# Optimization experiments

Measured on AMD Instinct MI355X. Metric: run time of the kernel, lower is better.

Reference implementation:

```python
import jax, jax.numpy as jnp
import numpy as np

IN_DIM = 1024
HIDDEN = 1024
NUM_HEAD = 16
HEAD_DIM = HIDDEN // NUM_HEAD
B, S = 4, 2048


def setup_inputs() -> dict:
    key = jax.random.key(0)
    ks = jax.random.split(key, 10)
    sc = 1.0 / np.sqrt(IN_DIM)
    inp = {
        "x": jax.random.normal(ks[0], (B, S, IN_DIM), dtype=jnp.float32),
        "mask": jnp.ones((B, 1, 1, S), dtype=jnp.int32),
        "Wq": jax.random.normal(ks[1], (IN_DIM, HIDDEN), dtype=jnp.float32) * sc,
        "bq": jnp.zeros((HIDDEN,), dtype=jnp.float32),
        "Wk": jax.random.normal(ks[2], (IN_DIM, HIDDEN), dtype=jnp.float32) * sc,
        "bk": jnp.zeros((HIDDEN,), dtype=jnp.float32),
        "Wv": jax.random.normal(ks[3], (IN_DIM, HIDDEN), dtype=jnp.float32) * sc,
        "bv": jnp.zeros((HIDDEN,), dtype=jnp.float32),
        "Wo": jax.random.normal(ks[4], (HIDDEN, IN_DIM), dtype=jnp.float32) * sc,
        "bo": jnp.zeros((IN_DIM,), dtype=jnp.float32),
    }
    return inp


def reference(x, mask, Wq, bq, Wk, bk, Wv, bv, Wo, bo):
    Bq, Sq, _ = x.shape
    # projections -> [B, H, S, hd]
    def proj(W, b):
        return (x @ W + b).reshape(Bq, Sq, NUM_HEAD, HEAD_DIM).transpose(0, 2, 1, 3)
    q, k, v = proj(Wq, bq), proj(Wk, bk), proj(Wv, bv)
    scale = 1.0 / jnp.sqrt(jnp.asarray(HEAD_DIM, dtype=x.dtype))
    scores = jnp.einsum("bhqd,bhkd->bhqk", q, k) * scale  # [B,H,S,S]
    scores = jnp.where(mask == 0, jnp.asarray(-1e9, dtype=x.dtype), scores)
    attn = jax.nn.softmax(scores, axis=-1)
    out = jnp.einsum("bhqk,bhkd->bhqd", attn, v)  # [B,H,S,hd]
    out = out.transpose(0, 2, 1, 3).reshape(Bq, Sq, HIDDEN)
    return out @ Wo + bo
```

## Files before the change

### kernel.cpp

```cpp
#include <hip/hip_runtime.h>
#include <hip/hip_bf16.h>
#include <stdint.h>

#define BB_ 4
#define SS_ 2048
#define IND_ 1024
#define HIDD_ 1024
#define NH_ 16
#define HD_ 64

typedef __attribute__((ext_vector_type(8))) short vshort8;
typedef __attribute__((ext_vector_type(4))) short vshort4;
typedef __attribute__((ext_vector_type(4))) float vfloat4;

__device__ __forceinline__ short bf16_of(float f) {
    union { float f; uint32_t u; } v; v.f = f;
    uint32_t r = v.u + 0x7fffu + ((v.u >> 16) & 1u);
    return (short)(r >> 16);
}

__device__ __forceinline__ uint32_t pk_bf16(float lo, float hi) {
    uint32_t r;
    asm("v_cvt_pk_bf16_f32 %0, %1, %2" : "=v"(r) : "v"(lo), "v"(hi));
    return r;
}

typedef const __attribute__((address_space(1))) uint8_t* gas_ptr;
typedef __attribute__((address_space(3))) uint8_t* las_ptr;
__device__ __forceinline__ void gload16(const void* g, void* l) {
    __builtin_amdgcn_global_load_lds((gas_ptr)g, (las_ptr)l, 16, 0, 0);
}

__global__ __launch_bounds__(256) void conv_x(const float* __restrict__ x,
                                              short* __restrict__ xb, int n4) {
    int i = blockIdx.x * 256 + threadIdx.x;
    if (i >= n4) return;
    float4 v = ((const float4*)x)[i];
    vshort4 r;
    r[0] = bf16_of(v.x); r[1] = bf16_of(v.y); r[2] = bf16_of(v.z); r[3] = bf16_of(v.w);
    ((vshort4*)xb)[i] = r;
}

__global__ __launch_bounds__(256) void convT_w4(const float* __restrict__ W0,
                                                const float* __restrict__ W1,
                                                const float* __restrict__ W2,
                                                const float* __restrict__ W3,
                                                short* __restrict__ T0,
                                                short* __restrict__ T1,
                                                short* __restrict__ T2,
                                                short* __restrict__ T3) {
    const float* W = (blockIdx.z == 0) ? W0 : (blockIdx.z == 1) ? W1 : (blockIdx.z == 2) ? W2 : W3;
    short* Wt = (blockIdx.z == 0) ? T0 : (blockIdx.z == 1) ? T1 : (blockIdx.z == 2) ? T2 : T3;
    __shared__ short tile[64][65];
    int k0 = blockIdx.x * 64, n0 = blockIdx.y * 64;
#pragma unroll
    for (int i = 0; i < 16; i++) {
        int idx = i * 256 + threadIdx.x;
        int r = idx >> 6, c = idx & 63;
        tile[c][r] = bf16_of(W[(k0 + r) * 1024 + n0 + c]);
    }
    __syncthreads();
#pragma unroll
    for (int i = 0; i < 16; i++) {
        int idx = i * 256 + threadIdx.x;
        int r = idx >> 6, c = idx & 63;
        Wt[(n0 + r) * 1024 + k0 + c] = tile[r][c];
    }
}

template <int MODE>
__device__ __forceinline__ void gemm_body(const short* __restrict__ A,
                                          const short* __restrict__ Bt,
                                          const float* __restrict__ bias,
                                          void* __restrict__ out, float scale,
                                          short* smem) {
    constexpr int Kd = 1024;
    const int t = threadIdx.x;
    const int w = t >> 6, lane = t & 63;
    const int g = lane >> 4, c = lane & 15;
    const int wm = w >> 1, wn = w & 1;
    const int m0 = blockIdx.x * 128, n0 = blockIdx.y * 128;

    const int row = t >> 2;
    const int colE = (t & 3) * 8;

    const short* ga0 = A + (size_t)(m0 + row) * Kd + colE;
    const short* ga1 = A + (size_t)(m0 + 64 + row) * Kd + colE;
    const short* gb0 = Bt + (size_t)(n0 + row) * Kd + colE;
    const short* gb1 = Bt + (size_t)(n0 + 64 + row) * Kd + colE;

    vfloat4 acc[4][4] = {};

    gload16(ga0, &smem[t * 8]);
    gload16(ga1, &smem[2048 + t * 8]);
    gload16(gb0, &smem[4096 + t * 8]);
    gload16(gb1, &smem[6144 + t * 8]);
    __syncthreads();

    for (int k0 = 0; k0 < Kd; k0 += 32) {
        const int cur = (k0 >> 5) & 1;
        const int nb = (cur ^ 1) * 8192;
        if (k0 + 32 < Kd) {
            gload16(ga0 + k0 + 32, &smem[nb + t * 8]);
            gload16(ga1 + k0 + 32, &smem[nb + 2048 + t * 8]);
            gload16(gb0 + k0 + 32, &smem[nb + 4096 + t * 8]);
            gload16(gb1 + k0 + 32, &smem[nb + 6144 + t * 8]);
        }
        const int cb = cur * 8192;
        vshort8 af[4], bfr[4];
#pragma unroll
        for (int mi = 0; mi < 4; mi++)
            af[mi] = *(const vshort8*)&smem[cb + (wm * 64 + mi * 16 + c) * 32 + g * 8];
#pragma unroll
        for (int ni = 0; ni < 4; ni++)
            bfr[ni] = *(const vshort8*)&smem[cb + 4096 + (wn * 64 + ni * 16 + c) * 32 + g * 8];
#pragma unroll
        for (int mi = 0; mi < 4; mi++)
#pragma unroll
            for (int ni = 0; ni < 4; ni++)
                acc[mi][ni] = __builtin_amdgcn_mfma_f32_16x16x32_bf16(
                    af[mi], bfr[ni], acc[mi][ni], 0, 0, 0);
        __syncthreads();
    }

#pragma unroll
    for (int ni = 0; ni < 4; ni++) {
        const int n = n0 + wn * 64 + ni * 16 + c;
        const float bv = bias[n];
#pragma unroll
        for (int mi = 0; mi < 4; mi++) {
#pragma unroll
            for (int r = 0; r < 4; r++) {
                const int m = m0 + wm * 64 + mi * 16 + g * 4 + r;
                const float v = (acc[mi][ni][r] + bv) * scale;
                if (MODE == 0) {
                    const int b = m >> 11, s = m & 2047, h = n >> 6, d = n & 63;
                    ((short*)out)[(((size_t)(b * 16 + h)) * 2048 + s) * 64 + d] = bf16_of(v);
                } else {
                    ((float*)out)[(size_t)m * 1024 + n] = v;
                }
            }
        }
    }
}

__global__ __launch_bounds__(256) void gemm_qkv(const short* __restrict__ xb,
                                                const short* __restrict__ Wqt,
                                                const short* __restrict__ Wkt,
                                                const short* __restrict__ Wvt,
                                                const float* __restrict__ bq,
                                                const float* __restrict__ bk,
                                                const float* __restrict__ bv,
                                                short* __restrict__ Qb,
                                                short* __restrict__ Kb,
                                                short* __restrict__ Vb) {
    __shared__ alignas(16) short smem[16384];
    const int z = blockIdx.z;
    const short* Bt = (z == 0) ? Wqt : (z == 1) ? Wkt : Wvt;
    const float* bias = (z == 0) ? bq : (z == 1) ? bk : bv;
    short* out = (z == 0) ? Qb : (z == 1) ? Kb : Vb;
    const float scale = (z == 0) ? 0.125f * 1.4426950408889634f : 1.0f;
    gemm_body<0>(xb, Bt, bias, out, scale, smem);
}

__global__ __launch_bounds__(256) void gemm_out(const short* __restrict__ A,
                                                const short* __restrict__ Bt,
                                                const float* __restrict__ bias,
                                                float* __restrict__ out) {
    __shared__ alignas(16) short smem[16384];
    gemm_body<1>(A, Bt, bias, out, 1.0f, smem);
}

__global__ __launch_bounds__(256) void transpose_v(const short* __restrict__ V,
                                                   short* __restrict__ Vt) {
    __shared__ short tile[64][65];
    const int bh = blockIdx.y;
    const int s0 = blockIdx.x * 64;
#pragma unroll
    for (int i = 0; i < 16; i++) {
        int idx = i * 256 + threadIdx.x;
        int r = idx >> 6, c = idx & 63;
        tile[c][r] = V[((size_t)bh * 2048 + s0 + r) * 64 + c];
    }
    __syncthreads();
#pragma unroll
    for (int i = 0; i < 16; i++) {
        int idx = i * 256 + threadIdx.x;
        int r = idx >> 6, c = idx & 63;
        Vt[((size_t)bh * 64 + r) * 2048 + s0 + c] = tile[r][c];
    }
}

__device__ __forceinline__ vshort8 lds_frag(const short* base, int row, int off) {
    const int byte = row * 128 + (off ^ ((row & 7) << 4));
    return *(const vshort8*)((const char*)base + byte);
}
__device__ __forceinline__ uint2 lds_frag8B(const short* base, int row, int eoff) {
    const int byte = row * 128 + ((eoff * 2) ^ ((row & 7) << 4));
    return *(const uint2*)((const char*)base + byte);
}
__device__ __forceinline__ void lds_stg(short* base, int row, int e8, vshort8 v) {
    const int byte = row * 128 + ((e8 * 16) ^ ((row & 7) << 4));
    *(vshort8*)((char*)base + byte) = v;
}

__global__ __launch_bounds__(256) void attn_kernel(const short* __restrict__ Q,
                                                   const short* __restrict__ K,
                                                   const short* __restrict__ Vt,
                                                   const int* __restrict__ mask,
                                                   short* __restrict__ Oattn) {
    __shared__ alignas(16) short Kl[2][64 * 64];
    __shared__ alignas(16) short Vl[2][64 * 64];
    const int tid = threadIdx.x, w = tid >> 6, lane = tid & 63;
    const int g = lane >> 4, c = lane & 15;
    const int bh = blockIdx.y, bb = bh >> 4, h = bh & 15;
    const int q0 = blockIdx.x * 128 + w * 32;
    const short* Qb = Q + (size_t)bh * 2048 * 64;
    const short* Kb = K + (size_t)bh * 2048 * 64;
    const short* Vb = Vt + (size_t)bh * 64 * 2048;
    const int* mb = mask + bb * 2048;

    const int srow = tid >> 3, se8 = tid & 7;
    const int srow2 = srow + 32;

    vshort8 qa[2][2];
#pragma unroll
    for (int qt = 0; qt < 2; qt++)
#pragma unroll
        for (int kf = 0; kf < 2; kf++)
            qa[qt][kf] = *(const vshort8*)(Qb + (size_t)(q0 + qt * 16 + c) * 64 + kf * 32 + g * 8);

    vfloat4 o[2][4] = {};
    vfloat4 osum[2] = {};
    const vfloat4 ZF = {0.f, 0.f, 0.f, 0.f};
    vshort8 ONESV;
#pragma unroll
    for (int i = 0; i < 8; i++) ONESV[i] = (short)0x3F80;

    vshort8 rk0 = *(const vshort8*)(Kb + (size_t)srow * 64 + se8 * 8);
    vshort8 rk1 = *(const vshort8*)(Kb + (size_t)srow2 * 64 + se8 * 8);
    vshort8 rv0 = *(const vshort8*)(Vb + (size_t)srow * 2048 + se8 * 8);
    vshort8 rv1 = *(const vshort8*)(Vb + (size_t)srow2 * 2048 + se8 * 8);
    lds_stg(Kl[0], srow, se8, rk0);
    lds_stg(Kl[0], srow2, se8, rk1);
    lds_stg(Vl[0], srow, se8, rv0);
    lds_stg(Vl[0], srow2, se8, rv1);
    __syncthreads();

    for (int t = 0; t < 32; t++) {
        const int k0 = t * 64;
        const short* Kc = Kl[t & 1];
        const short* Vc = Vl[t & 1];
        const bool more = (t + 1 < 32);
        if (more) {
            const int kn = k0 + 64;
            rk0 = *(const vshort8*)(Kb + (size_t)(kn + srow) * 64 + se8 * 8);
            rk1 = *(const vshort8*)(Kb + (size_t)(kn + srow2) * 64 + se8 * 8);
            rv0 = *(const vshort8*)(Vb + (size_t)srow * 2048 + kn + se8 * 8);
            rv1 = *(const vshort8*)(Vb + (size_t)srow2 * 2048 + kn + se8 * 8);
        }

        const int mv = mb[k0 + lane];
        const bool allone = __all(mv != 0);

        vshort8 kb[4][2];
#pragma unroll
        for (int kt = 0; kt < 4; kt++) {
            kb[kt][0] = lds_frag(Kc, kt * 16 + c, g * 16);
            kb[kt][1] = lds_frag(Kc, kt * 16 + c, 64 + g * 16);
        }
        vfloat4 s[2][4];
        __builtin_amdgcn_s_setprio(1);
#pragma unroll
        for (int qt = 0; qt < 2; qt++)
#pragma unroll
            for (int kt = 0; kt < 4; kt++) {
                vfloat4 z = __builtin_amdgcn_mfma_f32_16x16x32_bf16(kb[kt][0], qa[qt][0], ZF, 0, 0, 0);
                s[qt][kt] = __builtin_amdgcn_mfma_f32_16x16x32_bf16(kb[kt][1], qa[qt][1], z, 0, 0, 0);
            }
        __builtin_amdgcn_s_setprio(0);

        if (!allone) {
#pragma unroll
            for (int kt = 0; kt < 4; kt++)
#pragma unroll
                for (int r = 0; r < 4; r++) {
                    if (mb[k0 + kt * 16 + g * 4 + r] == 0) {
                        s[0][kt][r] = -3e8f;
                        s[1][kt][r] = -3e8f;
                    }
                }
        }

#pragma unroll
        for (int qt = 0; qt < 2; qt++)
#pragma unroll
            for (int kt = 0; kt < 4; kt++)
#pragma unroll
                for (int r = 0; r < 4; r++)
                    s[qt][kt][r] = exp2f(s[qt][kt][r]);

        __builtin_amdgcn_s_setprio(1);
#pragma unroll
        for (int u = 0; u < 2; u++) {
            union { uint32_t uu[4]; vshort8 v; } Pf[2];
#pragma unroll
            for (int qt = 0; qt < 2; qt++) {
                Pf[qt].uu[0] = pk_bf16(s[qt][2 * u][0], s[qt][2 * u][1]);
                Pf[qt].uu[1] = pk_bf16(s[qt][2 * u][2], s[qt][2 * u][3]);
                Pf[qt].uu[2] = pk_bf16(s[qt][2 * u + 1][0], s[qt][2 * u + 1][1]);
                Pf[qt].uu[3] = pk_bf16(s[qt][2 * u + 1][2], s[qt][2 * u + 1][3]);
            }
            const int e0 = (2 * u) * 16 + g * 4;
            const int e1 = (2 * u + 1) * 16 + g * 4;
#pragma unroll
            for (int dt = 0; dt < 4; dt++) {
                const uint2 x0 = lds_frag8B(Vc, dt * 16 + c, e0);
                const uint2 x1 = lds_frag8B(Vc, dt * 16 + c, e1);
                union { uint32_t uu[4]; vshort8 v; } Vf;
                Vf.uu[0] = x0.x; Vf.uu[1] = x0.y; Vf.uu[2] = x1.x; Vf.uu[3] = x1.y;
                o[0][dt] = __builtin_amdgcn_mfma_f32_16x16x32_bf16(Pf[0].v, Vf.v, o[0][dt], 0, 0, 0);
                o[1][dt] = __builtin_amdgcn_mfma_f32_16x16x32_bf16(Pf[1].v, Vf.v, o[1][dt], 0, 0, 0);
            }
            osum[0] = __builtin_amdgcn_mfma_f32_16x16x32_bf16(Pf[0].v, ONESV, osum[0], 0, 0, 0);
            osum[1] = __builtin_amdgcn_mfma_f32_16x16x32_bf16(Pf[1].v, ONESV, osum[1], 0, 0, 0);
        }
        __builtin_amdgcn_s_setprio(0);

        if (more) {
            short* Kn = Kl[(t + 1) & 1];
            short* Vn = Vl[(t + 1) & 1];
            lds_stg(Kn, srow, se8, rk0);
            lds_stg(Kn, srow2, se8, rk1);
            lds_stg(Vn, srow, se8, rv0);
            lds_stg(Vn, srow2, se8, rv1);
            __syncthreads();
        }
    }

#pragma unroll
    for (int qt = 0; qt < 2; qt++)
#pragma unroll
        for (int r = 0; r < 4; r++) {
            const float inv = 1.0f / osum[qt][r];
            const int q = q0 + qt * 16 + g * 4 + r;
#pragma unroll
            for (int dt = 0; dt < 4; dt++) {
                const float v = o[qt][dt][r] * inv;
                Oattn[((size_t)bb * 2048 + q) * 1024 + h * 64 + dt * 16 + c] = bf16_of(v);
            }
        }
}

extern "C" void kernel_launch(void* const* d_in, const int* in_sizes, int n_in,
                              void* d_out, int out_size, void* d_ws, size_t ws_size,
                              hipStream_t stream) {
    const float* x   = (const float*)d_in[0];
    const int*  mask = (const int*)d_in[1];
    const float* Wq  = (const float*)d_in[2];
    const float* bq  = (const float*)d_in[3];
    const float* Wk  = (const float*)d_in[4];
    const float* bk  = (const float*)d_in[5];
    const float* Wv  = (const float*)d_in[6];
    const float* bv  = (const float*)d_in[7];
    const float* Wo  = (const float*)d_in[8];
    const float* bo  = (const float*)d_in[9];
    float* out = (float*)d_out;

    short* xb  = (short*)d_ws;
    short* Wqt = xb + 8192 * 1024;
    short* Wkt = Wqt + 1024 * 1024;
    short* Wvt = Wkt + 1024 * 1024;
    short* Wot = Wvt + 1024 * 1024;
    short* Qb  = Wot + 1024 * 1024;
    short* Kb  = Qb + 8192 * 1024;
    short* Vb  = Kb + 8192 * 1024;
    short* Vtb = Vb + 8192 * 1024;
    short* att = Vtb + 8192 * 1024;

    conv_x<<<8192, 256, 0, stream>>>(x, xb, 8192 * 1024 / 4);
    convT_w4<<<dim3(16, 16, 4), 256, 0, stream>>>(Wq, Wk, Wv, Wo, Wqt, Wkt, Wvt, Wot);

    gemm_qkv<<<dim3(64, 8, 3), 256, 0, stream>>>(xb, Wqt, Wkt, Wvt, bq, bk, bv, Qb, Kb, Vb);

    transpose_v<<<dim3(32, 64), 256, 0, stream>>>(Vb, Vtb);
    attn_kernel<<<dim3(16, 64), 256, 0, stream>>>(Qb, Kb, Vtb, mask, att);

    gemm_out<<<dim3(64, 8), 256, 0, stream>>>(att, Wot, bo, out);
}
```

Baseline: 221.6 us.

## Fuse V transpose into QKV GEMM epilogue and widen attention blocks to 512 threads

The V projection epilogue now stages its tile in shared memory with an XOR swizzle and writes V already transposed as [B,H,D,S], so the separate transpose_v kernel and its extra round trip through global memory are gone. The attention kernel moves to 512-thread blocks covering 256 queries, so each K/V tile loaded into LDS is shared by twice as many waves and each thread issues one load per tile instead of two. In exchange there are fewer blocks per grid, more LDS pressure per block, and a new epilogue path whose indexing has to be correct.

```diff
diff --git a/kernel.cpp b/kernel.cpp
--- a/kernel.cpp
+++ b/kernel.cpp
@@ -123,21 +123,48 @@
         __syncthreads();
     }
 
-#pragma unroll
-    for (int ni = 0; ni < 4; ni++) {
-        const int n = n0 + wn * 64 + ni * 16 + c;
-        const float bv = bias[n];
-#pragma unroll
-        for (int mi = 0; mi < 4; mi++) {
-#pragma unroll
-            for (int r = 0; r < 4; r++) {
-                const int m = m0 + wm * 64 + mi * 16 + g * 4 + r;
-                const float v = (acc[mi][ni][r] + bv) * scale;
-                if (MODE == 0) {
-                    const int b = m >> 11, s = m & 2047, h = n >> 6, d = n & 63;
-                    ((short*)out)[(((size_t)(b * 16 + h)) * 2048 + s) * 64 + d] = bf16_of(v);
-                } else {
-                    ((float*)out)[(size_t)m * 1024 + n] = v;
+    if (MODE == 2) {
+        short* st = smem;
+#pragma unroll
+        for (int ni = 0; ni < 4; ni++) {
+            const int nl = wn * 64 + ni * 16 + c;
+            const float bv = bias[n0 + nl];
+            const int sx = (nl & 15) << 3;
+#pragma unroll
+            for (int mi = 0; mi < 4; mi++) {
+#pragma unroll
+                for (int r = 0; r < 4; r++) {
+                    const int ml = wm * 64 + mi * 16 + g * 4 + r;
+                    st[nl * 128 + (ml ^ sx)] = bf16_of((acc[mi][ni][r] + bv) * scale);
+                }
+            }
+        }
+        __syncthreads();
+        const int nl = t >> 1, hb = (t & 1) * 8;
+        const int n = n0 + nl, hh = n >> 6, d = n & 63;
+        const int b = m0 >> 11, s0l = m0 & 2047;
+        short* dst = (short*)out + (((size_t)(b * 16 + hh)) * 64 + d) * 2048 + s0l + (t & 1) * 64;
+        const vshort8* srcrow = (const vshort8*)&st[nl * 128];
+#pragma unroll
+        for (int j = 0; j < 8; j++)
+            ((vshort8*)dst)[j] = srcrow[(hb + j) ^ (nl & 15)];
+    } else {
+#pragma unroll
+        for (int ni = 0; ni < 4; ni++) {
+            const int n = n0 + wn * 64 + ni * 16 + c;
+            const float bv = bias[n];
+#pragma unroll
+            for (int mi = 0; mi < 4; mi++) {
+#pragma unroll
+                for (int r = 0; r < 4; r++) {
+                    const int m = m0 + wm * 64 + mi * 16 + g * 4 + r;
+                    const float v = (acc[mi][ni][r] + bv) * scale;
+                    if (MODE == 0) {
+                        const int b = m >> 11, s = m & 2047, h = n >> 6, d = n & 63;
+                        ((short*)out)[(((size_t)(b * 16 + h)) * 2048 + s) * 64 + d] = bf16_of(v);
+                    } else {
+                        ((float*)out)[(size_t)m * 1024 + n] = v;
+                    }
                 }
             }
         }
@@ -153,14 +180,16 @@
                                                 const float* __restrict__ bv,
                                                 short* __restrict__ Qb,
                                                 short* __restrict__ Kb,
-                                                short* __restrict__ Vb) {
+                                                short* __restrict__ Vtb) {
     __shared__ alignas(16) short smem[16384];
     const int z = blockIdx.z;
-    const short* Bt = (z == 0) ? Wqt : (z == 1) ? Wkt : Wvt;
-    const float* bias = (z == 0) ? bq : (z == 1) ? bk : bv;
-    short* out = (z == 0) ? Qb : (z == 1) ? Kb : Vb;
-    const float scale = (z == 0) ? 0.125f * 1.4426950408889634f : 1.0f;
-    gemm_body<0>(xb, Bt, bias, out, scale, smem);
+    if (z == 2) {
+        gemm_body<2>(xb, Wvt, bv, Vtb, 1.0f, smem);
+    } else if (z == 1) {
+        gemm_body<0>(xb, Wkt, bk, Kb, 1.0f, smem);
+    } else {
+        gemm_body<0>(xb, Wqt, bq, Qb, 0.125f * 1.4426950408889634f, smem);
+    }
 }
 
 __global__ __launch_bounds__(256) void gemm_out(const short* __restrict__ A,
@@ -171,26 +200,6 @@
     gemm_body<1>(A, Bt, bias, out, 1.0f, smem);
 }
 
-__global__ __launch_bounds__(256) void transpose_v(const short* __restrict__ V,
-                                                   short* __restrict__ Vt) {
-    __shared__ short tile[64][65];
-    const int bh = blockIdx.y;
-    const int s0 = blockIdx.x * 64;
-#pragma unroll
-    for (int i = 0; i < 16; i++) {
-        int idx = i * 256 + threadIdx.x;
-        int r = idx >> 6, c = idx & 63;
-        tile[c][r] = V[((size_t)bh * 2048 + s0 + r) * 64 + c];
-    }
-    __syncthreads();
-#pragma unroll
-    for (int i = 0; i < 16; i++) {
-        int idx = i * 256 + threadIdx.x;
-        int r = idx >> 6, c = idx & 63;
-        Vt[((size_t)bh * 64 + r) * 2048 + s0 + c] = tile[r][c];
-    }
-}
-
 __device__ __forceinline__ vshort8 lds_frag(const short* base, int row, int off) {
     const int byte = row * 128 + (off ^ ((row & 7) << 4));
     return *(const vshort8*)((const char*)base + byte);
@@ -204,7 +213,7 @@
     *(vshort8*)((char*)base + byte) = v;
 }
 
-__global__ __launch_bounds__(256) void attn_kernel(const short* __restrict__ Q,
+__global__ __launch_bounds__(512) void attn_kernel(const short* __restrict__ Q,
                                                    const short* __restrict__ K,
                                                    const short* __restrict__ Vt,
                                                    const int* __restrict__ mask,
@@ -214,14 +223,13 @@
     const int tid = threadIdx.x, w = tid >> 6, lane = tid & 63;
     const int g = lane >> 4, c = lane & 15;
     const int bh = blockIdx.y, bb = bh >> 4, h = bh & 15;
-    const int q0 = blockIdx.x * 128 + w * 32;
+    const int q0 = blockIdx.x * 256 + w * 32;
     const short* Qb = Q + (size_t)bh * 2048 * 64;
     const short* Kb = K + (size_t)bh * 2048 * 64;
     const short* Vb = Vt + (size_t)bh * 64 * 2048;
     const int* mb = mask + bb * 2048;
 
     const int srow = tid >> 3, se8 = tid & 7;
-    const int srow2 = srow + 32;
 
     vshort8 qa[2][2];
 #pragma unroll
@@ -237,14 +245,10 @@
 #pragma unroll
     for (int i = 0; i < 8; i++) ONESV[i] = (short)0x3F80;
 
-    vshort8 rk0 = *(const vshort8*)(Kb + (size_t)srow * 64 + se8 * 8);
-    vshort8 rk1 = *(const vshort8*)(Kb + (size_t)srow2 * 64 + se8 * 8);
-    vshort8 rv0 = *(const vshort8*)(Vb + (size_t)srow * 2048 + se8 * 8);
-    vshort8 rv1 = *(const vshort8*)(Vb + (size_t)srow2 * 2048 + se8 * 8);
-    lds_stg(Kl[0], srow, se8, rk0);
-    lds_stg(Kl[0], srow2, se8, rk1);
-    lds_stg(Vl[0], srow, se8, rv0);
-    lds_stg(Vl[0], srow2, se8, rv1);
+    vshort8 rk = *(const vshort8*)(Kb + (size_t)srow * 64 + se8 * 8);
+    vshort8 rv = *(const vshort8*)(Vb + (size_t)srow * 2048 + se8 * 8);
+    lds_stg(Kl[0], srow, se8, rk);
+    lds_stg(Vl[0], srow, se8, rv);
     __syncthreads();
 
     for (int t = 0; t < 32; t++) {
@@ -254,10 +258,8 @@
         const bool more = (t + 1 < 32);
         if (more) {
             const int kn = k0 + 64;
-            rk0 = *(const vshort8*)(Kb + (size_t)(kn + srow) * 64 + se8 * 8);
-            rk1 = *(const vshort8*)(Kb + (size_t)(kn + srow2) * 64 + se8 * 8);
-            rv0 = *(const vshort8*)(Vb + (size_t)srow * 2048 + kn + se8 * 8);
-            rv1 = *(const vshort8*)(Vb + (size_t)srow2 * 2048 + kn + se8 * 8);
+            rk = *(const vshort8*)(Kb + (size_t)(kn + srow) * 64 + se8 * 8);
+            rv = *(const vshort8*)(Vb + (size_t)srow * 2048 + kn + se8 * 8);
         }
 
         const int mv = mb[k0 + lane];
@@ -328,12 +330,8 @@
         __builtin_amdgcn_s_setprio(0);
 
         if (more) {
-            short* Kn = Kl[(t + 1) & 1];
-            short* Vn = Vl[(t + 1) & 1];
-            lds_stg(Kn, srow, se8, rk0);
-            lds_stg(Kn, srow2, se8, rk1);
-            lds_stg(Vn, srow, se8, rv0);
-            lds_stg(Vn, srow2, se8, rv1);
+            lds_stg(Kl[(t + 1) & 1], srow, se8, rk);
+            lds_stg(Vl[(t + 1) & 1], srow, se8, rv);
             __syncthreads();
         }
     }
@@ -381,10 +379,9 @@
     conv_x<<<8192, 256, 0, stream>>>(x, xb, 8192 * 1024 / 4);
     convT_w4<<<dim3(16, 16, 4), 256, 0, stream>>>(Wq, Wk, Wv, Wo, Wqt, Wkt, Wvt, Wot);
 
-    gemm_qkv<<<dim3(64, 8, 3), 256, 0, stream>>>(xb, Wqt, Wkt, Wvt, bq, bk, bv, Qb, Kb, Vb);
-
-    transpose_v<<<dim3(32, 64), 256, 0, stream>>>(Vb, Vtb);
-    attn_kernel<<<dim3(16, 64), 256, 0, stream>>>(Qb, Kb, Vtb, mask, att);
+    gemm_qkv<<<dim3(64, 8, 3), 256, 0, stream>>>(xb, Wqt, Wkt, Wvt, bq, bk, bv, Qb, Kb, Vtb);
+
+    attn_kernel<<<dim3(8, 64), 512, 0, stream>>>(Qb, Kb, Vtb, mask, att);
 
     gemm_out<<<dim3(64, 8), 256, 0, stream>>>(att, Wot, bo, out);
 }
```

Measured after the change: 223.3 us. No clear change (+0.8%).
